# Kernel optimization log

Measured on AMD Instinct MI355X. Metric: run time of the kernel, lower is better.

## Reference

```python
import jax, jax.numpy as jnp
import numpy as np

HEADS = 8
D_MODEL = 512
D_K = D_MODEL // HEADS


def setup_inputs() -> dict:
    key = jax.random.key(0)
    ks = jax.random.split(key, 12)
    B, S = 2, 4096
    scale = 1.0 / np.sqrt(D_MODEL)
    inp = {
        "q": jax.random.normal(ks[0], (B, S, D_MODEL), jnp.float32),
        "k": jax.random.normal(ks[1], (B, S, D_MODEL), jnp.float32),
        "v": jax.random.normal(ks[2], (B, S, D_MODEL), jnp.float32),
        "mask": jax.random.randint(ks[3], (B, 1, 1, S), 0, 2, jnp.int32),
        "wq": jax.random.normal(ks[4], (D_MODEL, D_MODEL), jnp.float32) * scale,
        "bq": jnp.zeros((D_MODEL,), jnp.float32),
        "wk": jax.random.normal(ks[5], (D_MODEL, D_MODEL), jnp.float32) * scale,
        "bk": jnp.zeros((D_MODEL,), jnp.float32),
        "wv": jax.random.normal(ks[6], (D_MODEL, D_MODEL), jnp.float32) * scale,
        "bv": jnp.zeros((D_MODEL,), jnp.float32),
        "wo": jax.random.normal(ks[7], (D_MODEL, D_MODEL), jnp.float32) * scale,
        "bo": jnp.zeros((D_MODEL,), jnp.float32),
    }
    return inp


def reference(q, k, v, mask, wq, bq, wk, bk, wv, bv, wo, bo):
    B, S, _ = q.shape
    # torch nn.Linear: y = x @ W.T + b
    qh = (q @ wq.T + bq).reshape(B, S, HEADS, D_K).transpose(0, 2, 1, 3)  # b h s d
    kh = (k @ wk.T + bk).reshape(B, S, HEADS, D_K).transpose(0, 2, 1, 3)
    vh = (v @ wv.T + bv).reshape(B, S, HEADS, D_K).transpose(0, 2, 1, 3)
    scores = jnp.einsum("bhqd,bhkd->bhqk", qh, kh) / jnp.sqrt(jnp.float32(D_K))
    scores = jnp.where(mask == 0, jnp.float32(-1e9), scores)
    attn = jax.nn.softmax(scores, axis=-1)  # dropout is identity in eval mode
    out = jnp.einsum("bhqk,bhkd->bhqd", attn, vh)
    out = out.transpose(0, 2, 1, 3).reshape(B, S, D_MODEL)
    return out @ wo.T + bo
```

## Files before the change

### kernel.cpp

```cpp
#include <hip/hip_runtime.h>
#include <hip/hip_bf16.h>

#define S 4096
#define DM 512
#define HH 8
#define DK 64
#define MT 8192
#define KVB 64

typedef __attribute__((ext_vector_type(8)))  short bf16x8;
typedef __attribute__((ext_vector_type(4)))  float f32x4;
typedef __attribute__((ext_vector_type(16))) float f32x16;
typedef __attribute__((ext_vector_type(4)))  unsigned int u32x4;

#define CQ 0.18033688011112042f

__device__ __forceinline__ short f2bs(float x) {
    __hip_bfloat16 h = __float2bfloat16(x);
    return *reinterpret_cast<short*>(&h);
}

__device__ __forceinline__ bf16x8 pack8(const float4& a, const float4& b) {
    bf16x8 r;
    r[0] = f2bs(a.x); r[1] = f2bs(a.y); r[2] = f2bs(a.z); r[3] = f2bs(a.w);
    r[4] = f2bs(b.x); r[5] = f2bs(b.y); r[6] = f2bs(b.z); r[7] = f2bs(b.w);
    return r;
}

__device__ __forceinline__ unsigned cvtpk(float lo, float hi) {
    unsigned r;
    asm("v_cvt_pk_bf16_f32 %0, %1, %2" : "=v"(r) : "v"(lo), "v"(hi));
    return r;
}

__device__ __forceinline__ bf16x8 mk_pb(unsigned a, unsigned b, unsigned c, unsigned d) {
    u32x4 t; t[0] = a; t[1] = b; t[2] = c; t[3] = d;
    return __builtin_bit_cast(bf16x8, t);
}

__global__ __launch_bounds__(256, 4)
void qkv_gemm(const float* __restrict__ Xq, const float* __restrict__ Xk,
              const float* __restrict__ Xv,
              const float* __restrict__ Wq, const float* __restrict__ Wk,
              const float* __restrict__ Wv,
              const float* __restrict__ Bq, const float* __restrict__ Bk,
              const float* __restrict__ Bv,
              unsigned short* __restrict__ Yq, unsigned short* __restrict__ Yk,
              unsigned short* __restrict__ Yv)
{
    __shared__ char As[128 * 128];
    __shared__ char Bs[64 * 128];
    const int bid  = blockIdx.x;
    const int work = (bid & 7) * 192 + (bid >> 3);
    const int gp   = work >> 3;
    const int mat  = gp >> 6;
    const int m0   = (gp & 63) * 128;
    const int n0   = (work & 7) * 64;
    const float* X    = mat == 0 ? Xq : (mat == 1 ? Xk : Xv);
    const float* W    = mat == 0 ? Wq : (mat == 1 ? Wk : Wv);
    const float* bias = mat == 0 ? Bq : (mat == 1 ? Bk : Bv);

    const int t = threadIdx.x, l = t & 63, w = t >> 6;
    const int wr = w >> 1, wc = w & 1;
    const int lr = l & 15, lg = l >> 4;
    const int srow = t >> 3, schk = t & 7;
    const int sswz = (schk ^ (srow & 7)) * 16;

    float4 fA[4][2]; float4 fB[2][2];
    auto loadA = [&](int k0) {
        #pragma unroll
        for (int i = 0; i < 4; ++i) {
            const float* p = X + (size_t)(m0 + srow + 32 * i) * DM + k0 + schk * 8;
            fA[i][0] = *(const float4*)p;
            fA[i][1] = *(const float4*)(p + 4);
        }
    };
    auto loadB = [&](int k0) {
        #pragma unroll
        for (int i = 0; i < 2; ++i) {
            const float* p = W + (size_t)(n0 + srow + 32 * i) * DM + k0 + schk * 8;
            fB[i][0] = *(const float4*)p;
            fB[i][1] = *(const float4*)(p + 4);
        }
    };

    loadA(0); loadB(0);

    f32x4 acc[4][2];
    #pragma unroll
    for (int fm = 0; fm < 4; ++fm)
        #pragma unroll
        for (int fn = 0; fn < 2; ++fn) acc[fm][fn] = f32x4{0.f, 0.f, 0.f, 0.f};

    #pragma unroll
    for (int kt = 0; kt < 8; ++kt) {
        bf16x8 wA[4], wB[2];
        #pragma unroll
        for (int i = 0; i < 4; ++i) wA[i] = pack8(fA[i][0], fA[i][1]);
        #pragma unroll
        for (int i = 0; i < 2; ++i) wB[i] = pack8(fB[i][0], fB[i][1]);

        if (kt < 7) { loadA((kt + 1) * 64); loadB((kt + 1) * 64); }

        __syncthreads();
        #pragma unroll
        for (int i = 0; i < 4; ++i)
            *(bf16x8*)(As + (srow + 32 * i) * 128 + sswz) = wA[i];
        #pragma unroll
        for (int i = 0; i < 2; ++i)
            *(bf16x8*)(Bs + (srow + 32 * i) * 128 + sswz) = wB[i];
        __syncthreads();

        #pragma unroll
        for (int kc = 0; kc < 2; ++kc) {
            bf16x8 af[4], bfr[2];
            #pragma unroll
            for (int fm = 0; fm < 4; ++fm) {
                int row = wr * 64 + fm * 16 + lr;
                af[fm] = *(const bf16x8*)(As + row * 128 + (((kc * 4 + lg) ^ (row & 7)) * 16));
            }
            #pragma unroll
            for (int fn = 0; fn < 2; ++fn) {
                int row = wc * 32 + fn * 16 + lr;
                bfr[fn] = *(const bf16x8*)(Bs + row * 128 + (((kc * 4 + lg) ^ (row & 7)) * 16));
            }
            #pragma unroll
            for (int fm = 0; fm < 4; ++fm)
                #pragma unroll
                for (int fn = 0; fn < 2; ++fn)
                    acc[fm][fn] = __builtin_amdgcn_mfma_f32_16x16x32_bf16(af[fm], bfr[fn], acc[fm][fn], 0, 0, 0);
        }
    }

    const float scale = (mat == 0) ? CQ : 1.0f;
    #pragma unroll
    for (int fm = 0; fm < 4; ++fm) {
        #pragma unroll
        for (int fn = 0; fn < 2; ++fn) {
            int n = n0 + wc * 32 + fn * 16 + lr;
            float bn = bias[n];
            int mbase = m0 + wr * 64 + fm * 16 + lg * 4;
            int h = n >> 6, d = n & 63;
            if (mat < 2) {
                unsigned short* Y = (mat == 0) ? Yq : Yk;
                #pragma unroll
                for (int r = 0; r < 4; ++r) {
                    int m = mbase + r, b = m >> 12, s = m & (S - 1);
                    Y[(((size_t)(b * HH + h)) * S + s) * DK + d] =
                        (unsigned short)f2bs((acc[fm][fn][r] + bn) * scale);
                }
            } else {
                int b = mbase >> 12, s = mbase & (S - 1);
                ushort4 u;
                u.x = (unsigned short)f2bs(acc[fm][fn][0] + bn);
                u.y = (unsigned short)f2bs(acc[fm][fn][1] + bn);
                u.z = (unsigned short)f2bs(acc[fm][fn][2] + bn);
                u.w = (unsigned short)f2bs(acc[fm][fn][3] + bn);
                *(ushort4*)(Yv + ((size_t)((b * HH + h) * DK + d)) * S + s) = u;
            }
        }
    }
}

__global__ __launch_bounds__(256, 2)
void out_gemm(const short* __restrict__ Xb, const float* __restrict__ W,
              const float* __restrict__ bias, float* __restrict__ Y)
{
    __shared__ char As[128 * 128];
    __shared__ char Bs[64 * 128];
    const int bid  = blockIdx.x;
    const int work = (bid & 7) * 64 + (bid >> 3);
    const int n0 = (work & 7) * 64;
    const int m0 = (work >> 3) * 128;

    const int t = threadIdx.x, l = t & 63, w = t >> 6;
    const int wr = w >> 1, wc = w & 1;
    const int lr = l & 15, lg = l >> 4;
    const int srow = t >> 3, schk = t & 7;
    const int sswz = (schk ^ (srow & 7)) * 16;

    float4 fB[2][2]; bf16x8 rA[4];
    auto loadA = [&](int k0) {
        #pragma unroll
        for (int i = 0; i < 4; ++i)
            rA[i] = *(const bf16x8*)(Xb + (size_t)(m0 + srow + 32 * i) * DM + k0 + schk * 8);
    };
    auto loadB = [&](int k0) {
        #pragma unroll
        for (int i = 0; i < 2; ++i) {
            const float* p = W + (size_t)(n0 + srow + 32 * i) * DM + k0 + schk * 8;
            fB[i][0] = *(const float4*)p;
            fB[i][1] = *(const float4*)(p + 4);
        }
    };

    loadA(0); loadB(0);

    f32x4 acc[4][2];
    #pragma unroll
    for (int fm = 0; fm < 4; ++fm)
        #pragma unroll
        for (int fn = 0; fn < 2; ++fn) acc[fm][fn] = f32x4{0.f, 0.f, 0.f, 0.f};

    #pragma unroll
    for (int kt = 0; kt < 8; ++kt) {
        bf16x8 wA[4], wB[2];
        #pragma unroll
        for (int i = 0; i < 4; ++i) wA[i] = rA[i];
        #pragma unroll
        for (int i = 0; i < 2; ++i) wB[i] = pack8(fB[i][0], fB[i][1]);

        if (kt < 7) { loadA((kt + 1) * 64); loadB((kt + 1) * 64); }

        __syncthreads();
        #pragma unroll
        for (int i = 0; i < 4; ++i)
            *(bf16x8*)(As + (srow + 32 * i) * 128 + sswz) = wA[i];
        #pragma unroll
        for (int i = 0; i < 2; ++i)
            *(bf16x8*)(Bs + (srow + 32 * i) * 128 + sswz) = wB[i];
        __syncthreads();

        #pragma unroll
        for (int kc = 0; kc < 2; ++kc) {
            bf16x8 af[4], bfr[2];
            #pragma unroll
            for (int fm = 0; fm < 4; ++fm) {
                int row = wr * 64 + fm * 16 + lr;
                af[fm] = *(const bf16x8*)(As + row * 128 + (((kc * 4 + lg) ^ (row & 7)) * 16));
            }
            #pragma unroll
            for (int fn = 0; fn < 2; ++fn) {
                int row = wc * 32 + fn * 16 + lr;
                bfr[fn] = *(const bf16x8*)(Bs + row * 128 + (((kc * 4 + lg) ^ (row & 7)) * 16));
            }
            #pragma unroll
            for (int fm = 0; fm < 4; ++fm)
                #pragma unroll
                for (int fn = 0; fn < 2; ++fn)
                    acc[fm][fn] = __builtin_amdgcn_mfma_f32_16x16x32_bf16(af[fm], bfr[fn], acc[fm][fn], 0, 0, 0);
        }
    }

    #pragma unroll
    for (int fm = 0; fm < 4; ++fm) {
        #pragma unroll
        for (int fn = 0; fn < 2; ++fn) {
            int n = n0 + wc * 32 + fn * 16 + lr;
            float bn = bias[n];
            int mbase = m0 + wr * 64 + fm * 16 + lg * 4;
            #pragma unroll
            for (int r = 0; r < 4; ++r)
                Y[(size_t)(mbase + r) * DM + n] = acc[fm][fn][r] + bn;
        }
    }
}

__global__ __launch_bounds__(256, 4)
void flash_mfma(const __hip_bfloat16* __restrict__ qh,
                const __hip_bfloat16* __restrict__ kh,
                const __hip_bfloat16* __restrict__ vt,
                const int* __restrict__ mask,
                __hip_bfloat16* __restrict__ att)
{
    const int bh = blockIdx.y, b = bh >> 3, h = bh & 7;
    const int q0 = blockIdx.x * 64;
    const int t = threadIdx.x, w = t >> 6, l = t & 63;
    const int l31 = l & 31, hi = l >> 5;
    const int kw = w & 1, qw = w >> 1;

    __shared__ char sBuf[32768 + 2 * KVB * 4];
    char* Ks0 = sBuf;
    char* Ks1 = sBuf + 8192;
    char* Vs0 = sBuf + 16384;
    char* Vs1 = sBuf + 24576;
    float* mskf = (float*)(sBuf + 32768);

    const short* qg = (const short*)qh + ((size_t)bh * S + q0 + qw * 32 + l31) * DK;
    bf16x8 qf[4];
    #pragma unroll
    for (int c = 0; c < 4; ++c)
        qf[c] = *(const bf16x8*)(qg + c * 16 + hi * 8);

    f32x16 oc[2];
    #pragma unroll
    for (int dt = 0; dt < 2; ++dt)
        #pragma unroll
        for (int r = 0; r < 16; ++r) oc[dt][r] = 0.f;
    float ls = 0.f;

    const int sr = t >> 2, c2 = (t & 3) * 2;
    const short* ksrc = (const short*)kh + (size_t)bh * S * DK + (size_t)sr * DK + c2 * 8;
    const short* vsrc = (const short*)vt + (size_t)bh * DK * S + (size_t)sr * S + c2 * 8;
    const int*   msrc = mask + b * S + (t & (KVB - 1));

    bf16x8 rK[2], rV[2];
    float  mreg = 0.f;

    auto issue = [&]() {
        rK[0] = *(const bf16x8*)(ksrc);
        rK[1] = *(const bf16x8*)(ksrc + 8);
        rV[0] = *(const bf16x8*)(vsrc);
        rV[1] = *(const bf16x8*)(vsrc + 8);
        if (t < KVB) mreg = msrc[0] ? 0.f : -3e38f;
        ksrc += KVB * DK; vsrc += KVB; msrc += KVB;
    };
    auto stageTo = [&](char* kb, char* vb, float* mf) {
        *(bf16x8*)(kb + sr * 128 + ((c2 ^ (sr & 7)) * 16))       = rK[0];
        *(bf16x8*)(kb + sr * 128 + (((c2 + 1) ^ (sr & 7)) * 16)) = rK[1];
        *(bf16x8*)(vb + sr * 128 + ((c2 ^ (sr & 7)) * 16))       = rV[0];
        *(bf16x8*)(vb + sr * 128 + (((c2 + 1) ^ (sr & 7)) * 16)) = rV[1];
        if (t < KVB) mf[t] = mreg;
    };

    const int kbase = kw * 32;
    const int kr    = kbase + l31;

    auto tile = [&](const char* kb, const char* vb, const float* mf) {
        f32x16 sc;
        #pragma unroll
        for (int g = 0; g < 4; ++g) {
            f32x4 m4 = *(const f32x4*)(mf + kbase + g * 8 + hi * 4);
            #pragma unroll
            for (int o = 0; o < 4; ++o) sc[g * 4 + o] = m4[o];
        }
        __builtin_amdgcn_s_setprio(1);
        #pragma unroll
        for (int c = 0; c < 4; ++c) {
            bf16x8 kf = *(const bf16x8*)(kb + kr * 128 + (((c * 2 + hi) ^ (kr & 7)) * 16));
            sc = __builtin_amdgcn_mfma_f32_32x32x16_bf16(kf, qf[c], sc, 0, 0, 0);
        }
        __builtin_amdgcn_s_setprio(0);

        float p[16];
        #pragma unroll
        for (int r = 0; r < 16; ++r) p[r] = exp2f(sc[r]);
        float a0 = 0.f;
        #pragma unroll
        for (int r = 0; r < 16; r += 4)
            a0 += (p[r] + p[r + 1]) + (p[r + 2] + p[r + 3]);
        ls += a0;

        unsigned A0 = cvtpk(p[0],  p[1]),  B0 = cvtpk(p[2],  p[3]);
        unsigned A1 = cvtpk(p[4],  p[5]),  B1 = cvtpk(p[6],  p[7]);
        unsigned A2 = cvtpk(p[8],  p[9]),  B2 = cvtpk(p[10], p[11]);
        unsigned A3 = cvtpk(p[12], p[13]), B3 = cvtpk(p[14], p[15]);
        asm("v_permlane32_swap_b32 %0, %1" : "+v"(A0), "+v"(A1));
        asm("v_permlane32_swap_b32 %0, %1" : "+v"(B0), "+v"(B1));
        asm("v_permlane32_swap_b32 %0, %1" : "+v"(A2), "+v"(A3));
        asm("v_permlane32_swap_b32 %0, %1" : "+v"(B2), "+v"(B3));
        bf16x8 pb0 = mk_pb(A0, B0, A1, B1);
        bf16x8 pb1 = mk_pb(A2, B2, A3, B3);

        __builtin_amdgcn_s_setprio(1);
        #pragma unroll
        for (int kcl = 0; kcl < 2; ++kcl) {
            const bf16x8 pb = kcl ? pb1 : pb0;
            #pragma unroll
            for (int dt = 0; dt < 2; ++dt) {
                const int vrow = dt * 32 + l31;
                bf16x8 vf = *(const bf16x8*)(vb + vrow * 128 +
                                (((kw * 4 + kcl * 2 + hi) ^ (vrow & 7)) * 16));
                oc[dt] = __builtin_amdgcn_mfma_f32_32x32x16_bf16(vf, pb, oc[dt], 0, 0, 0);
            }
        }
        __builtin_amdgcn_s_setprio(0);
    };

    const int NT = S / KVB;
    issue(); stageTo(Ks0, Vs0, mskf); issue();

    for (int it2 = 0; it2 < NT / 2; ++it2) {
        const int it = it2 * 2;
        __syncthreads();
        stageTo(Ks1, Vs1, mskf + KVB);
        if (it < NT - 2) issue();
        tile(Ks0, Vs0, mskf);
        __syncthreads();
        if (it + 1 < NT - 1) stageTo(Ks0, Vs0, mskf);
        if (it + 1 < NT - 2) issue();
        tile(Ks1, Vs1, mskf + KVB);
    }

    __syncthreads();
    float* scr = (float*)sBuf;
    float* pp  = scr + (size_t)(qw * 64 + l) * 33;
    if (kw == 1) {
        #pragma unroll
        for (int r = 0; r < 16; ++r) { pp[r] = oc[0][r]; pp[16 + r] = oc[1][r]; }
        pp[32] = ls;
    }
    __syncthreads();
    if (kw == 0) {
        #pragma unroll
        for (int r = 0; r < 16; ++r) { oc[0][r] += pp[r]; oc[1][r] += pp[16 + r]; }
        ls += pp[32];
        ls += __shfl_xor(ls, 32);
        const float linv = 1.0f / ls;
        unsigned short* ap = (unsigned short*)att +
            ((size_t)(b * S + q0 + qw * 32 + l31)) * DM + h * DK;
        #pragma unroll
        for (int dt = 0; dt < 2; ++dt)
            #pragma unroll
            for (int g = 0; g < 4; ++g) {
                uint2 u;
                u.x = cvtpk(oc[dt][g * 4 + 0] * linv, oc[dt][g * 4 + 1] * linv);
                u.y = cvtpk(oc[dt][g * 4 + 2] * linv, oc[dt][g * 4 + 3] * linv);
                *(uint2*)(ap + dt * 32 + g * 8 + hi * 4) = u;
            }
    }
}

extern "C" void kernel_launch(void* const* d_in, const int* in_sizes, int n_in,
                              void* d_out, int out_size, void* d_ws, size_t ws_size,
                              hipStream_t stream) {
    const float* q    = (const float*)d_in[0];
    const float* k    = (const float*)d_in[1];
    const float* v    = (const float*)d_in[2];
    const int*   mask = (const int*)  d_in[3];
    const float* wq   = (const float*)d_in[4];
    const float* bq   = (const float*)d_in[5];
    const float* wk   = (const float*)d_in[6];
    const float* bk   = (const float*)d_in[7];
    const float* wv   = (const float*)d_in[8];
    const float* bv   = (const float*)d_in[9];
    const float* wo   = (const float*)d_in[10];
    const float* bo   = (const float*)d_in[11];
    float* out = (float*)d_out;

    char* wsb = (char*)d_ws;
    __hip_bfloat16* qh  = (__hip_bfloat16*)(wsb);
    __hip_bfloat16* kh  = (__hip_bfloat16*)(wsb + (size_t)8  * 1024 * 1024);
    __hip_bfloat16* vt  = (__hip_bfloat16*)(wsb + (size_t)16 * 1024 * 1024);
    __hip_bfloat16* att = (__hip_bfloat16*)(wsb + (size_t)24 * 1024 * 1024);

    dim3 blk(256);
    qkv_gemm<<<dim3(1536), blk, 0, stream>>>(q, k, v, wq, wk, wv, bq, bk, bv,
                                     (unsigned short*)qh, (unsigned short*)kh,
                                     (unsigned short*)vt);

    dim3 g2(S / 64, 16);
    flash_mfma<<<g2, blk, 0, stream>>>(qh, kh, vt, mask, att);

    out_gemm<<<dim3(512), blk, 0, stream>>>((const short*)att, wo, bo, out);
}
```

Before: 166.7 us.

## Load K/V fragments directly from global memory in flash kernel, drop LDS staging

The flash attention kernel no longer stages K and V tiles through double-buffered shared memory with block-wide barriers. Each lane now loads its MFMA fragments straight from global memory (relying on L2/cache reuse), and the mask is converted once to additive float form inside the QKV GEMM and written to workspace. This removes LDS write/read traffic and two __syncthreads per tile pair. In exchange the loads are less coalesced, there is no explicit prefetch to hide global latency, and K/V are re-fetched by every wave instead of shared.

```diff
diff --git a/kernel.cpp b/kernel.cpp
--- a/kernel.cpp
+++ b/kernel.cpp
@@ -6,7 +6,6 @@
 #define HH 8
 #define DK 64
 #define MT 8192
-#define KVB 64
 
 typedef __attribute__((ext_vector_type(8)))  short bf16x8;
 typedef __attribute__((ext_vector_type(4)))  float f32x4;
@@ -45,12 +44,18 @@
               const float* __restrict__ Wv,
               const float* __restrict__ Bq, const float* __restrict__ Bk,
               const float* __restrict__ Bv,
+              const int* __restrict__ mask, float* __restrict__ maskf,
               unsigned short* __restrict__ Yq, unsigned short* __restrict__ Yk,
               unsigned short* __restrict__ Yv)
 {
     __shared__ char As[128 * 128];
     __shared__ char Bs[64 * 128];
     const int bid  = blockIdx.x;
+    const int t = threadIdx.x;
+    if (bid < 32) {
+        int i = bid * 256 + t;
+        maskf[i] = mask[i] ? 0.f : -3e38f;
+    }
     const int work = (bid & 7) * 192 + (bid >> 3);
     const int gp   = work >> 3;
     const int mat  = gp >> 6;
@@ -60,7 +65,7 @@
     const float* W    = mat == 0 ? Wq : (mat == 1 ? Wk : Wv);
     const float* bias = mat == 0 ? Bq : (mat == 1 ? Bk : Bv);
 
-    const int t = threadIdx.x, l = t & 63, w = t >> 6;
+    const int l = t & 63, w = t >> 6;
     const int wr = w >> 1, wc = w & 1;
     const int lr = l & 15, lg = l >> 4;
     const int srow = t >> 3, schk = t & 7;
@@ -260,7 +265,7 @@
 void flash_mfma(const __hip_bfloat16* __restrict__ qh,
                 const __hip_bfloat16* __restrict__ kh,
                 const __hip_bfloat16* __restrict__ vt,
-                const int* __restrict__ mask,
+                const float* __restrict__ maskf,
                 __hip_bfloat16* __restrict__ att)
 {
     const int bh = blockIdx.y, b = bh >> 3, h = bh & 7;
@@ -269,12 +274,7 @@
     const int l31 = l & 31, hi = l >> 5;
     const int kw = w & 1, qw = w >> 1;
 
-    __shared__ char sBuf[32768 + 2 * KVB * 4];
-    char* Ks0 = sBuf;
-    char* Ks1 = sBuf + 8192;
-    char* Vs0 = sBuf + 16384;
-    char* Vs1 = sBuf + 24576;
-    float* mskf = (float*)(sBuf + 32768);
+    __shared__ float scr[2 * 64 * 33];
 
     const short* qg = (const short*)qh + ((size_t)bh * S + q0 + qw * 32 + l31) * DK;
     bf16x8 qf[4];
@@ -289,48 +289,38 @@
         for (int r = 0; r < 16; ++r) oc[dt][r] = 0.f;
     float ls = 0.f;
 
-    const int sr = t >> 2, c2 = (t & 3) * 2;
-    const short* ksrc = (const short*)kh + (size_t)bh * S * DK + (size_t)sr * DK + c2 * 8;
-    const short* vsrc = (const short*)vt + (size_t)bh * DK * S + (size_t)sr * S + c2 * 8;
-    const int*   msrc = mask + b * S + (t & (KVB - 1));
-
-    bf16x8 rK[2], rV[2];
-    float  mreg = 0.f;
-
-    auto issue = [&]() {
-        rK[0] = *(const bf16x8*)(ksrc);
-        rK[1] = *(const bf16x8*)(ksrc + 8);
-        rV[0] = *(const bf16x8*)(vsrc);
-        rV[1] = *(const bf16x8*)(vsrc + 8);
-        if (t < KVB) mreg = msrc[0] ? 0.f : -3e38f;
-        ksrc += KVB * DK; vsrc += KVB; msrc += KVB;
-    };
-    auto stageTo = [&](char* kb, char* vb, float* mf) {
-        *(bf16x8*)(kb + sr * 128 + ((c2 ^ (sr & 7)) * 16))       = rK[0];
-        *(bf16x8*)(kb + sr * 128 + (((c2 + 1) ^ (sr & 7)) * 16)) = rK[1];
-        *(bf16x8*)(vb + sr * 128 + ((c2 ^ (sr & 7)) * 16))       = rV[0];
-        *(bf16x8*)(vb + sr * 128 + (((c2 + 1) ^ (sr & 7)) * 16)) = rV[1];
-        if (t < KVB) mf[t] = mreg;
-    };
-
-    const int kbase = kw * 32;
-    const int kr    = kbase + l31;
-
-    auto tile = [&](const char* kb, const char* vb, const float* mf) {
+    const short* kp = (const short*)kh + (size_t)bh * S * DK +
+                      (size_t)(kw * 32 + l31) * DK + hi * 8;
+    const short* vp = (const short*)vt + (size_t)bh * DK * S +
+                      (size_t)l31 * S + kw * 32 + hi * 8;
+    const float* mp = maskf + b * S + kw * 32 + hi * 4;
+
+    for (int step = 0; step < S / 64; ++step) {
+        f32x4 m40 = *(const f32x4*)(mp);
+        f32x4 m41 = *(const f32x4*)(mp + 8);
+        f32x4 m42 = *(const f32x4*)(mp + 16);
+        f32x4 m43 = *(const f32x4*)(mp + 24);
+        bf16x8 kf0 = *(const bf16x8*)(kp);
+        bf16x8 kf1 = *(const bf16x8*)(kp + 16);
+        bf16x8 kf2 = *(const bf16x8*)(kp + 32);
+        bf16x8 kf3 = *(const bf16x8*)(kp + 48);
         f32x16 sc;
         #pragma unroll
-        for (int g = 0; g < 4; ++g) {
-            f32x4 m4 = *(const f32x4*)(mf + kbase + g * 8 + hi * 4);
-            #pragma unroll
-            for (int o = 0; o < 4; ++o) sc[g * 4 + o] = m4[o];
+        for (int o = 0; o < 4; ++o) {
+            sc[o] = m40[o]; sc[4 + o] = m41[o];
+            sc[8 + o] = m42[o]; sc[12 + o] = m43[o];
         }
         __builtin_amdgcn_s_setprio(1);
-        #pragma unroll
-        for (int c = 0; c < 4; ++c) {
-            bf16x8 kf = *(const bf16x8*)(kb + kr * 128 + (((c * 2 + hi) ^ (kr & 7)) * 16));
-            sc = __builtin_amdgcn_mfma_f32_32x32x16_bf16(kf, qf[c], sc, 0, 0, 0);
-        }
+        sc = __builtin_amdgcn_mfma_f32_32x32x16_bf16(kf0, qf[0], sc, 0, 0, 0);
+        sc = __builtin_amdgcn_mfma_f32_32x32x16_bf16(kf1, qf[1], sc, 0, 0, 0);
+        sc = __builtin_amdgcn_mfma_f32_32x32x16_bf16(kf2, qf[2], sc, 0, 0, 0);
+        sc = __builtin_amdgcn_mfma_f32_32x32x16_bf16(kf3, qf[3], sc, 0, 0, 0);
         __builtin_amdgcn_s_setprio(0);
+
+        bf16x8 vf00 = *(const bf16x8*)(vp);
+        bf16x8 vf01 = *(const bf16x8*)(vp + 16);
+        bf16x8 vf10 = *(const bf16x8*)(vp + (size_t)32 * S);
+        bf16x8 vf11 = *(const bf16x8*)(vp + (size_t)32 * S + 16);
 
         float p[16];
         #pragma unroll
@@ -353,38 +343,17 @@
         bf16x8 pb1 = mk_pb(A2, B2, A3, B3);
 
         __builtin_amdgcn_s_setprio(1);
-        #pragma unroll
-        for (int kcl = 0; kcl < 2; ++kcl) {
-            const bf16x8 pb = kcl ? pb1 : pb0;
-            #pragma unroll
-            for (int dt = 0; dt < 2; ++dt) {
-                const int vrow = dt * 32 + l31;
-                bf16x8 vf = *(const bf16x8*)(vb + vrow * 128 +
-                                (((kw * 4 + kcl * 2 + hi) ^ (vrow & 7)) * 16));
-                oc[dt] = __builtin_amdgcn_mfma_f32_32x32x16_bf16(vf, pb, oc[dt], 0, 0, 0);
-            }
-        }
+        oc[0] = __builtin_amdgcn_mfma_f32_32x32x16_bf16(vf00, pb0, oc[0], 0, 0, 0);
+        oc[1] = __builtin_amdgcn_mfma_f32_32x32x16_bf16(vf10, pb0, oc[1], 0, 0, 0);
+        oc[0] = __builtin_amdgcn_mfma_f32_32x32x16_bf16(vf01, pb1, oc[0], 0, 0, 0);
+        oc[1] = __builtin_amdgcn_mfma_f32_32x32x16_bf16(vf11, pb1, oc[1], 0, 0, 0);
         __builtin_amdgcn_s_setprio(0);
-    };
-
-    const int NT = S / KVB;
-    issue(); stageTo(Ks0, Vs0, mskf); issue();
-
-    for (int it2 = 0; it2 < NT / 2; ++it2) {
-        const int it = it2 * 2;
-        __syncthreads();
-        stageTo(Ks1, Vs1, mskf + KVB);
-        if (it < NT - 2) issue();
-        tile(Ks0, Vs0, mskf);
-        __syncthreads();
-        if (it + 1 < NT - 1) stageTo(Ks0, Vs0, mskf);
-        if (it + 1 < NT - 2) issue();
-        tile(Ks1, Vs1, mskf + KVB);
+
+        kp += 64 * DK; vp += 64; mp += 64;
     }
 
     __syncthreads();
-    float* scr = (float*)sBuf;
-    float* pp  = scr + (size_t)(qw * 64 + l) * 33;
+    float* pp = scr + (size_t)(qw * 64 + l) * 33;
     if (kw == 1) {
         #pragma unroll
         for (int r = 0; r < 16; ++r) { pp[r] = oc[0][r]; pp[16 + r] = oc[1][r]; }
@@ -429,18 +398,20 @@
     float* out = (float*)d_out;
 
     char* wsb = (char*)d_ws;
-    __hip_bfloat16* qh  = (__hip_bfloat16*)(wsb);
-    __hip_bfloat16* kh  = (__hip_bfloat16*)(wsb + (size_t)8  * 1024 * 1024);
-    __hip_bfloat16* vt  = (__hip_bfloat16*)(wsb + (size_t)16 * 1024 * 1024);
-    __hip_bfloat16* att = (__hip_bfloat16*)(wsb + (size_t)24 * 1024 * 1024);
+    __hip_bfloat16* qh    = (__hip_bfloat16*)(wsb);
+    __hip_bfloat16* kh    = (__hip_bfloat16*)(wsb + (size_t)8  * 1024 * 1024);
+    __hip_bfloat16* vt    = (__hip_bfloat16*)(wsb + (size_t)16 * 1024 * 1024);
+    __hip_bfloat16* att   = (__hip_bfloat16*)(wsb + (size_t)24 * 1024 * 1024);
+    float*          maskf = (float*)         (wsb + (size_t)32 * 1024 * 1024);
 
     dim3 blk(256);
     qkv_gemm<<<dim3(1536), blk, 0, stream>>>(q, k, v, wq, wk, wv, bq, bk, bv,
+                                     mask, maskf,
                                      (unsigned short*)qh, (unsigned short*)kh,
                                      (unsigned short*)vt);
 
     dim3 g2(S / 64, 16);
-    flash_mfma<<<g2, blk, 0, stream>>>(qh, kh, vt, mask, att);
+    flash_mfma<<<g2, blk, 0, stream>>>(qh, kh, vt, maskf, att);
 
     out_gemm<<<dim3(512), blk, 0, stream>>>((const short*)att, wo, bo, out);
 }
```

After: 303.6 us. 1.82x slower.
